# Kernel tuning notes

Measured on AMD Instinct MI355X. Metric: run time of the kernel, lower is better.

The kernel has to match this reference:

```python
import jax, jax.numpy as jnp
import numpy as np
import math

PHI = (1 + math.sqrt(5)) / 2
COMPRESS_EXP = 2.0 / 3.0
ALPHA_D = 0.01


def c_mag(z):
    return jnp.sqrt(z[..., 0] ** 2 + z[..., 1] ** 2 + 1e-08)


def c_phase(z):
    return jnp.arctan2(z[..., 1], z[..., 0] + 1e-10)


def c_mul(a, b):
    real = a[..., 0] * b[..., 0] - a[..., 1] * b[..., 1]
    imag = a[..., 0] * b[..., 1] + a[..., 1] * b[..., 0]
    return jnp.stack([real, imag], axis=-1)


@jax.custom_vjp
def fractal_compress(mag):
    return jnp.clip(mag, 1e-08) ** COMPRESS_EXP


def _fc_fwd(mag):
    ms = jnp.clip(mag, 1e-08)
    c = ms ** COMPRESS_EXP
    return c, c / (ms + 1e-06)


def _fc_bwd(ratio, g):
    return (g * jnp.minimum(ratio, 2.0),)


fractal_compress.defvjp(_fc_fwd, _fc_bwd)


def converge(z):
    mag = c_mag(z)
    phase = c_phase(z)
    cm = fractal_compress(mag)
    return jnp.stack([cm * jnp.cos(phase), cm * jnp.sin(phase)], axis=-1)


def setup_inputs():
    key = jax.random.key(0)
    Bsz, T, D, S = 4, 512, 1024, 16
    dt_rank = D // 16
    ks = jax.random.split(key, 8)
    scale = 1.0 / PHI

    def u(k, shape):
        fan_in = shape[1]
        lim = scale / math.sqrt(fan_in)
        return jax.random.uniform(k, shape, minval=-lim, maxval=lim, dtype=jnp.float32)

    return {
        "x": jax.random.normal(ks[0], (Bsz, T, D), dtype=jnp.float32),
        "W_in": u(ks[1], (2 * D, D)),
        "W_xproj": u(ks[2], (dt_rank + 4 * S, D)),
        "W_dt": u(ks[3], (D, dt_rank)),
        "b_dt": jax.random.uniform(ks[4], (D,), minval=-0.1, maxval=0.1, dtype=jnp.float32),
        "W_out": u(ks[5], (D, D)),
        "b_out": jax.random.uniform(ks[6], (D,), minval=-0.1, maxval=0.1, dtype=jnp.float32),
        "W_res": u(ks[7], (2 * S, D)),
        "A_log": jnp.log(jnp.linspace(1.0, float(S), S)),
    }


def reference(x, W_in, W_xproj, W_dt, b_dt, W_out, b_out, W_res, A_log):
    Bsz, T, D = x.shape
    S = A_log.shape[0]
    dt_rank = W_dt.shape[1]

    xz = x @ W_in.T                      # [B,T,2D]
    x_in, z = xz[..., :D], xz[..., D:]
    x_in = jax.nn.silu(x_in)
    xp = x_in @ W_xproj.T                # [B,T,dt_rank+4S]
    dt = jax.nn.softplus(xp[..., :dt_rank] @ W_dt.T + b_dt)   # [B,T,D]
    bc = xp[..., dt_rank:].reshape(Bsz, T, 2, S, 2)
    B_all, C_all = bc[:, :, 0], bc[:, :, 1]                    # [B,T,S,2]

    A_neg = -jnp.exp(A_log)              # [S]

    # initial deep state d: differentiated phases, tiny magnitude
    phases = jnp.linspace(0.0, 2 * math.pi * (1 - 1.0 / S), S)
    d0 = jnp.stack([0.01 * jnp.cos(phases), 0.01 * jnp.sin(phases)], axis=-1)
    d0 = jnp.broadcast_to(d0, (Bsz, S, 2)).astype(x.dtype)
    h0 = jnp.zeros((Bsz, D, S, 2), dtype=x.dtype)

    def step(carry, xs):
        h_prev, d_prev = carry
        x_t, dt_t, B_t, C_t = xs        # [B,D], [B,D], [B,S,2], [B,S,2]
        x_complex = (x_t @ W_res.T).reshape(Bsz, S, 2)
        d_read = jax.lax.stop_gradient(d_prev)
        T_gate = jnp.cos((c_phase(x_complex) - c_phase(d_read)) / 2) ** 2  # [B,S]
        d_mag = c_mag(d_read)[..., None]
        d_normed = d_read / (d_mag + 1e-08)
        d_scale = jnp.sqrt(jnp.clip(d_mag, 1e-06, 20.0))
        surfaced = d_normed * d_scale * T_gate[..., None]                  # [B,S,2]

        alpha = jnp.exp(dt_t[..., None] * A_neg)                           # [B,D,S]
        x_full = jnp.stack([x_t, jnp.zeros_like(x_t)], axis=-1)            # [B,D,2]
        Bx = c_mul(B_t[:, None, :, :], x_full[:, :, None, :])              # [B,D,S,2]
        Bx = Bx + surfaced[:, None, :, :]
        Bx = Bx * dt_t[:, :, None, None]                                   # gamma scaling

        h_decayed = h_prev * alpha[..., None]
        released = h_prev * (1.0 - alpha)[..., None]
        comp = jnp.clip(converge(released), -10.0, 10.0)
        comp_avg = comp.mean(axis=1)                                       # [B,S,2]
        d_t = jax.lax.stop_gradient(d_prev) + ALPHA_D * comp_avg
        d_mag_new = c_mag(d_t)[..., None]
        d_t = jnp.where(d_mag_new > 20.0, d_t * (20.0 / d_mag_new), d_t)

        h_t = h_decayed + Bx
        Ch = c_mul(C_t[:, None, :, :], h_t)                                # [B,D,S,2]
        y_t = Ch[..., 0].sum(axis=-1)                                      # [B,D]
        return (h_t, d_t), y_t

    xs = (
        jnp.swapaxes(x_in, 0, 1),
        jnp.swapaxes(dt, 0, 1),
        jnp.swapaxes(B_all, 0, 1),
        jnp.swapaxes(C_all, 0, 1),
    )
    (_, _), ys = jax.lax.scan(step, (h0, d0), xs)
    y = jnp.swapaxes(ys, 0, 1)           # [B,T,D]
    y = y * jax.nn.silu(z)
    return y @ W_out.T + b_out
```

## Files before the change

kernel.cpp:

```cpp
#include <hip/hip_runtime.h>
#include <hip/hip_bf16.h>
#include <math.h>


enum { EPI_NONE=0, EPI_SILU=1, EPI_SPBIAS=2, EPI_BIAS=3 };

template<int EPI>
__device__ __forceinline__ float epi_apply(float v, float b) {
  if constexpr (EPI == EPI_SILU)        { return v / (1.0f + expf(-v)); }
  else if constexpr (EPI == EPI_SPBIAS) { float t = v + b; return fmaxf(t, 0.0f) + log1pf(expf(-fabsf(t))); }
  else if constexpr (EPI == EPI_BIAS)   { return v + b; }
  else return v;
}

template<int EPI, bool HAS_A2>
__global__ __launch_bounds__(256) void gemm_wt(
    const float* __restrict__ A, int lda,
    const float* __restrict__ A2, int lda2,
    const float* __restrict__ W, int ldw,
    const float* __restrict__ bias,
    float* __restrict__ C, int ldc,
    int N, int K)
{
  constexpr int BM = 64, BN = 64, BK = 32, PAD = 4;
  __shared__ float As[BK][BM + PAD];
  __shared__ float Ws[BK][BN + PAD];
  const int m0 = blockIdx.x * BM;
  const int n0 = blockIdx.y * BN;
  const int tid = threadIdx.x;
  const int tx = tid & 15;
  const int ty = tid >> 4;
  const int lm = tid & 63;
  const int lk = (tid >> 6) << 3;

  float4 a0, a1, w0, w1;
  {
    const float* p = A + (size_t)(m0 + lm) * lda + lk;
    a0 = ((const float4*)p)[0]; a1 = ((const float4*)p)[1];
    if (HAS_A2) {
      const float* p2 = A2 + (size_t)(m0 + lm) * lda2 + lk;
      const float4 b0 = ((const float4*)p2)[0], b1 = ((const float4*)p2)[1];
      a0.x*=b0.x; a0.y*=b0.y; a0.z*=b0.z; a0.w*=b0.w;
      a1.x*=b1.x; a1.y*=b1.y; a1.z*=b1.z; a1.w*=b1.w;
    }
    const int n = n0 + lm;
    if (n < N) {
      const float* pw = W + (size_t)n * ldw + lk;
      w0 = ((const float4*)pw)[0]; w1 = ((const float4*)pw)[1];
    } else { w0 = make_float4(0.f,0.f,0.f,0.f); w1 = w0; }
  }

  float acc[4][4] = {{0.f,0.f,0.f,0.f},{0.f,0.f,0.f,0.f},{0.f,0.f,0.f,0.f},{0.f,0.f,0.f,0.f}};
  const int NT = K / BK;

  for (int i = 0; i < NT; ++i) {
    __syncthreads();
    As[lk+0][lm]=a0.x; As[lk+1][lm]=a0.y; As[lk+2][lm]=a0.z; As[lk+3][lm]=a0.w;
    As[lk+4][lm]=a1.x; As[lk+5][lm]=a1.y; As[lk+6][lm]=a1.z; As[lk+7][lm]=a1.w;
    Ws[lk+0][lm]=w0.x; Ws[lk+1][lm]=w0.y; Ws[lk+2][lm]=w0.z; Ws[lk+3][lm]=w0.w;
    Ws[lk+4][lm]=w1.x; Ws[lk+5][lm]=w1.y; Ws[lk+6][lm]=w1.z; Ws[lk+7][lm]=w1.w;
    __syncthreads();
    if (i + 1 < NT) {
      const int k0 = (i + 1) * BK;
      const float* p = A + (size_t)(m0 + lm) * lda + k0 + lk;
      a0 = ((const float4*)p)[0]; a1 = ((const float4*)p)[1];
      if (HAS_A2) {
        const float* p2 = A2 + (size_t)(m0 + lm) * lda2 + k0 + lk;
        const float4 b0 = ((const float4*)p2)[0], b1 = ((const float4*)p2)[1];
        a0.x*=b0.x; a0.y*=b0.y; a0.z*=b0.z; a0.w*=b0.w;
        a1.x*=b1.x; a1.y*=b1.y; a1.z*=b1.z; a1.w*=b1.w;
      }
      const int n = n0 + lm;
      if (n < N) {
        const float* pw = W + (size_t)n * ldw + k0 + lk;
        w0 = ((const float4*)pw)[0]; w1 = ((const float4*)pw)[1];
      } else { w0 = make_float4(0.f,0.f,0.f,0.f); w1 = w0; }
    }
#pragma unroll
    for (int kk = 0; kk < BK; ++kk) {
      const float4 a = *(const float4*)&As[kk][ty << 2];
      const float4 w = *(const float4*)&Ws[kk][tx << 2];
      const float ar[4] = {a.x, a.y, a.z, a.w};
      const float wr[4] = {w.x, w.y, w.z, w.w};
#pragma unroll
      for (int ii = 0; ii < 4; ++ii)
#pragma unroll
        for (int j = 0; j < 4; ++j)
          acc[ii][j] = fmaf(ar[ii], wr[j], acc[ii][j]);
    }
  }

  const int ncol = n0 + (tx << 2);
  float bj[4] = {0.f, 0.f, 0.f, 0.f};
  if constexpr (EPI == EPI_SPBIAS || EPI == EPI_BIAS) {
    if (ncol < N) { const float4 bv = *(const float4*)(bias + ncol); bj[0]=bv.x; bj[1]=bv.y; bj[2]=bv.z; bj[3]=bv.w; }
  }
  if (ncol < N) {
#pragma unroll
    for (int i = 0; i < 4; ++i) {
      float vs[4];
#pragma unroll
      for (int j = 0; j < 4; ++j) vs[j] = epi_apply<EPI>(acc[i][j], bj[j]);
      *(float4*)(C + (size_t)(m0 + (ty << 2) + i) * ldc + ncol) = make_float4(vs[0], vs[1], vs[2], vs[3]);
    }
  }
}

__global__ __launch_bounds__(256) void gemm_dualw32(
    const float* __restrict__ A, int lda,
    const float* __restrict__ W1,
    const float* __restrict__ W2, int ldw,
    float* __restrict__ C, int ldc, int K)
{
  constexpr int BM = 32, BN = 32, BK = 32, PAD = 4;
  __shared__ float As[BK][BM + PAD];
  __shared__ float Ws[BK][BN + PAD];
  const int m0 = blockIdx.x * BM;
  const int n0 = blockIdx.y * BN;
  const int tid = threadIdx.x;
  const int tx = tid & 15;
  const int ty = tid >> 4;
  const int lm = tid & 31;
  const int lk = (tid >> 5) << 2;

  const int n = n0 + lm;
  const float* wrow = (n < 128) ? (W1 + (size_t)n * ldw) : (W2 + (size_t)(n - 128) * ldw);

  float4 av = *(const float4*)(A + (size_t)(m0 + lm) * lda + lk);
  float4 wv = *(const float4*)(wrow + lk);

  float acc[2][2] = {{0.f,0.f},{0.f,0.f}};
  const int NT = K / BK;
  for (int i = 0; i < NT; ++i) {
    __syncthreads();
    As[lk+0][lm]=av.x; As[lk+1][lm]=av.y; As[lk+2][lm]=av.z; As[lk+3][lm]=av.w;
    Ws[lk+0][lm]=wv.x; Ws[lk+1][lm]=wv.y; Ws[lk+2][lm]=wv.z; Ws[lk+3][lm]=wv.w;
    __syncthreads();
    if (i + 1 < NT) {
      const int k0 = (i + 1) * BK;
      av = *(const float4*)(A + (size_t)(m0 + lm) * lda + k0 + lk);
      wv = *(const float4*)(wrow + k0 + lk);
    }
#pragma unroll
    for (int kk = 0; kk < BK; ++kk) {
      const float2 a = *(const float2*)&As[kk][ty << 1];
      const float2 w = *(const float2*)&Ws[kk][tx << 1];
      acc[0][0] = fmaf(a.x, w.x, acc[0][0]);
      acc[0][1] = fmaf(a.x, w.y, acc[0][1]);
      acc[1][0] = fmaf(a.y, w.x, acc[1][0]);
      acc[1][1] = fmaf(a.y, w.y, acc[1][1]);
    }
  }
  const int ncol = n0 + (tx << 1);
  float* pc = C + (size_t)(m0 + (ty << 1)) * ldc + ncol;
  *(float2*)pc         = make_float2(acc[0][0], acc[0][1]);
  *(float2*)(pc + ldc) = make_float2(acc[1][0], acc[1][1]);
}

__global__ __launch_bounds__(256) void gemm_dt64(
    const float* __restrict__ A, int lda,
    const float* __restrict__ W,
    const float* __restrict__ bias,
    float* __restrict__ C, int ldc)
{
  __shared__ float As[64][68];
  __shared__ float Ws[64][68];
  const int m0 = blockIdx.x * 64;
  const int n0 = blockIdx.y * 64;
  const int tid = threadIdx.x;
  const int lm = tid & 63;
  const int kq = (tid >> 6) << 4;

  {
    const float* pa = A + (size_t)(m0 + lm) * lda + kq;
    const float4 a0 = ((const float4*)pa)[0];
    const float4 a1 = ((const float4*)pa)[1];
    const float4 a2 = ((const float4*)pa)[2];
    const float4 a3 = ((const float4*)pa)[3];
    const float* pw = W + (size_t)(n0 + lm) * 64 + kq;
    const float4 w0 = ((const float4*)pw)[0];
    const float4 w1 = ((const float4*)pw)[1];
    const float4 w2 = ((const float4*)pw)[2];
    const float4 w3 = ((const float4*)pw)[3];
    As[kq+ 0][lm]=a0.x; As[kq+ 1][lm]=a0.y; As[kq+ 2][lm]=a0.z; As[kq+ 3][lm]=a0.w;
    As[kq+ 4][lm]=a1.x; As[kq+ 5][lm]=a1.y; As[kq+ 6][lm]=a1.z; As[kq+ 7][lm]=a1.w;
    As[kq+ 8][lm]=a2.x; As[kq+ 9][lm]=a2.y; As[kq+10][lm]=a2.z; As[kq+11][lm]=a2.w;
    As[kq+12][lm]=a3.x; As[kq+13][lm]=a3.y; As[kq+14][lm]=a3.z; As[kq+15][lm]=a3.w;
    Ws[kq+ 0][lm]=w0.x; Ws[kq+ 1][lm]=w0.y; Ws[kq+ 2][lm]=w0.z; Ws[kq+ 3][lm]=w0.w;
    Ws[kq+ 4][lm]=w1.x; Ws[kq+ 5][lm]=w1.y; Ws[kq+ 6][lm]=w1.z; Ws[kq+ 7][lm]=w1.w;
    Ws[kq+ 8][lm]=w2.x; Ws[kq+ 9][lm]=w2.y; Ws[kq+10][lm]=w2.z; Ws[kq+11][lm]=w2.w;
    Ws[kq+12][lm]=w3.x; Ws[kq+13][lm]=w3.y; Ws[kq+14][lm]=w3.z; Ws[kq+15][lm]=w3.w;
  }
  __syncthreads();

  const int tx = tid & 15;
  const int ty = tid >> 4;
  float acc[4][4] = {{0.f,0.f,0.f,0.f},{0.f,0.f,0.f,0.f},{0.f,0.f,0.f,0.f},{0.f,0.f,0.f,0.f}};
#pragma unroll 16
  for (int kk = 0; kk < 64; ++kk) {
    const float4 a = *(const float4*)&As[kk][ty << 2];
    const float4 w = *(const float4*)&Ws[kk][tx << 2];
    const float ar[4] = {a.x, a.y, a.z, a.w};
    const float wr[4] = {w.x, w.y, w.z, w.w};
#pragma unroll
    for (int i = 0; i < 4; ++i)
#pragma unroll
      for (int j = 0; j < 4; ++j)
        acc[i][j] = fmaf(ar[i], wr[j], acc[i][j]);
  }

  const int ncol = n0 + (tx << 2);
  const float4 bv = *(const float4*)(bias + ncol);
  const float bj[4] = {bv.x, bv.y, bv.z, bv.w};
#pragma unroll
  for (int i = 0; i < 4; ++i) {
    float vs[4];
#pragma unroll
    for (int j = 0; j < 4; ++j) vs[j] = epi_apply<EPI_SPBIAS>(acc[i][j], bj[j]);
    *(float4*)(C + (size_t)(m0 + (ty << 2) + i) * ldc + ncol) = make_float4(vs[0], vs[1], vs[2], vs[3]);
  }
}

__global__ void zero_kernel(float4* __restrict__ p, int n4) {
  const int i = blockIdx.x * blockDim.x + threadIdx.x;
  if (i < n4) p[i] = make_float4(0.f, 0.f, 0.f, 0.f);
}

__global__ __launch_bounds__(256) void reduce_y_silu(
    const float4* __restrict__ yp, const float* __restrict__ siluxz,
    float4* __restrict__ yo, int n4)
{
  const int i = blockIdx.x * blockDim.x + threadIdx.x;
  if (i >= n4) return;
  float4 a = yp[i];
#pragma unroll
  for (int s = 1; s < 16; ++s) {
    const float4 v = yp[(size_t)s * 524288 + i];
    a.x += v.x; a.y += v.y; a.z += v.z; a.w += v.w;
  }
  const int row = i >> 8;
  const int c4  = i & 255;
  const float4 z = *(const float4*)(siluxz + (size_t)row * 2048 + 1024 + (c4 << 2));
  a.x *= z.x; a.y *= z.y; a.z *= z.z; a.w *= z.w;
  yo[i] = a;
}

__global__ __launch_bounds__(256) void mul_silu(
    float* __restrict__ y, const float* __restrict__ siluxz, int n)
{
  const int i = blockIdx.x * blockDim.x + threadIdx.x;
  if (i >= n) return;
  const int row = i >> 10;
  const int col = i & 1023;
  y[i] *= siluxz[(size_t)row * 2048 + 1024 + col];
}

template<int CTRL>
__device__ __forceinline__ float dpp_fadd(float x) {
  const int s = __builtin_amdgcn_update_dpp(0, __float_as_int(x), CTRL, 0xF, 0xF, true);
  return x + __int_as_float(s);
}
__device__ __forceinline__ float wave64_sum_l63(float x) {
  x = dpp_fadd<0x111>(x);
  x = dpp_fadd<0x112>(x);
  x = dpp_fadd<0x114>(x);
  x = dpp_fadd<0x118>(x);
  x = dpp_fadd<0x142>(x);
  x = dpp_fadd<0x143>(x);
  return x;
}

__device__ __forceinline__ void comp_block(const float4& dtv, const float na2,
    const float (&h_r)[4], const float (&h_i)[4], float (&al_out)[4],
    float& wr, float& wi)
{
  const float ta[4] = {dtv.x, dtv.y, dtv.z, dtv.w};
  float sr = 0.f, si = 0.f;
#pragma unroll
  for (int e = 0; e < 4; ++e) {
    const float a = exp2f(ta[e] * na2);
    al_out[e] = a;
    const float om    = 1.0f - a;
    const float rel_r = h_r[e] * om, rel_i = h_i[e] * om;
    const float m2 = fmaf(rel_r, rel_r, fmaf(rel_i, rel_i, 1e-8f));
    const float u  = exp2f(log2f(m2) * (-1.0f / 6.0f));
    const float rr = rel_r + 1e-10f;
    float cr = rr * u;    cr = fminf(fmaxf(cr, -10.f), 10.f);
    float ci = rel_i * u; ci = fminf(fmaxf(ci, -10.f), 10.f);
    sr += cr; si += ci;
  }
  wr = wave64_sum_l63(sr);
  wi = wave64_sum_l63(si);
}

template<bool PARTIAL>
__device__ __forceinline__ void step_update(
    float& d_r, float& d_i, const float avg_r, const float avg_i,
    const float2& cx, const float4& xv, const float4& dtv,
    const float2& Bv, const float2& Cv,
    const float (&alv)[4], float (&h_r)[4], float (&h_i)[4],
    float* py)
{
  d_r = fmaf(0.01f, avg_r, d_r);
  d_i = fmaf(0.01f, avg_i, d_i);
  const float dm2c = fmaf(d_r, d_r, fmaf(d_i, d_i, 1e-8f));
  if (dm2c > 400.f) { const float sc = 20.f * __builtin_amdgcn_rsqf(dm2c); d_r *= sc; d_i *= sc; }

  const float xr2 = cx.x + 1e-10f;
  const float irx = __builtin_amdgcn_rsqf(fmaf(xr2, xr2, fmaf(cx.y, cx.y, 1e-38f)));
  const float dr2 = d_r + 1e-10f;
  const float ird = __builtin_amdgcn_rsqf(fmaf(dr2, dr2, fmaf(d_i, d_i, 1e-38f)));
  const float cosdp = fmaf(xr2, dr2, cx.y * d_i) * irx * ird;
  const float Tg  = 0.5f * (1.0f + cosdp);
  const float md2 = fmaf(d_r, d_r, fmaf(d_i, d_i, 1e-8f));
  const float sf  = Tg * exp2f(log2f(md2) * -0.25f);
  const float s_r = d_r * sf, s_i = d_i * sf;

  const float xa[4] = {xv.x, xv.y, xv.z, xv.w};
  const float ta[4] = {dtv.x, dtv.y, dtv.z, dtv.w};
  float yv[4];
#pragma unroll
  for (int e = 0; e < 4; ++e) {
    const float bx_r = fmaf(Bv.x, xa[e], s_r) * ta[e];
    const float bx_i = fmaf(Bv.y, xa[e], s_i) * ta[e];
    h_r[e] = fmaf(h_r[e], alv[e], bx_r);
    h_i[e] = fmaf(h_i[e], alv[e], bx_i);
    yv[e] = fmaf(Cv.x, h_r[e], -(Cv.y * h_i[e]));
  }
  if (PARTIAL) {
    *(float4*)py = make_float4(yv[0], yv[1], yv[2], yv[3]);
  } else {
#pragma unroll
    for (int e = 0; e < 4; ++e) atomicAdd(py + e, yv[e]);
  }
}

template<int RB, int RO, bool PARTIAL>
__device__ __forceinline__ void period_body(
    const float* __restrict__ px, const float* __restrict__ pdt,
    const float* __restrict__ pB, const float* __restrict__ pC,
    const float* __restrict__ pxc, float* __restrict__ py,
    const float na2, const int lane, const int wid,
    float (*red)[4][4],
    float& d_r, float& d_i,
    float (&h_r)[4], float (&h_i)[4], float (&al)[4],
    float4& x0, float4& t0, float2& B0, float2& C0, float2& c0,
    float4& x1, float4& t1, float2& B1, float2& C1, float2& c1,
    const float4& t2)
{
  const float4 qa = *(const float4*)&red[RB][0][0];
  const float4 qb = *(const float4*)&red[RB][1][0];
  const float4 qc = *(const float4*)&red[RB][2][0];
  const float4 qd = *(const float4*)&red[RB][3][0];

  step_update<PARTIAL>(d_r, d_i,
      (qa.x + qb.x + qc.x + qd.x) * (1.0f / 1024.0f),
      (qa.y + qb.y + qc.y + qd.y) * (1.0f / 1024.0f),
      c0, x0, t0, B0, C0, al, h_r, h_i, py + (size_t)RO * 1024);

  x0 = *(const float4*)(px  + (size_t)(RO + 3) * 2048);
  t0 = *(const float4*)(pdt + (size_t)(RO + 3) * 1024);
  B0 = *(const float2*)(pB  + (RO + 3) * 160);
  C0 = *(const float2*)(pC  + (RO + 3) * 160);
  c0 = *(const float2*)(pxc + (RO + 3) * 160);

  float al1[4], w1r, w1i;
  comp_block(t1, na2, h_r, h_i, al1, w1r, w1i);

  step_update<PARTIAL>(d_r, d_i,
      (qa.z + qb.z + qc.z + qd.z) * (1.0f / 1024.0f),
      (qa.w + qb.w + qc.w + qd.w) * (1.0f / 1024.0f),
      c1, x1, t1, B1, C1, al1, h_r, h_i, py + (size_t)(RO + 1) * 1024);

  x1 = *(const float4*)(px  + (size_t)(RO + 4) * 2048);
  t1 = *(const float4*)(pdt + (size_t)(RO + 4) * 1024);
  B1 = *(const float2*)(pB  + (RO + 4) * 160);
  C1 = *(const float2*)(pC  + (RO + 4) * 160);
  c1 = *(const float2*)(pxc + (RO + 4) * 160);

  float w2r, w2i;
  comp_block(t2, na2, h_r, h_i, al, w2r, w2i);

  if (lane == 63) *(float4*)&red[(RB + 1) % 3][wid][0] = make_float4(w1r, w1i, w2r, w2i);

  asm volatile("s_waitcnt lgkmcnt(0)" ::: "memory");
  __builtin_amdgcn_s_barrier();
  asm volatile("" ::: "memory");
}

template<bool PARTIAL>
__global__ __launch_bounds__(256) void scan_g1b(
    const float* __restrict__ xin,
    const float* __restrict__ xpc,
    const float* __restrict__ dtb,
    const float* __restrict__ A_log,
    float* __restrict__ ybase,
    int T,
    const float* __restrict__ xg,
    const float* __restrict__ Wz,
    float* __restrict__ Cz)
{
  if (blockIdx.x < 64) {
    __builtin_amdgcn_s_setprio(1);

    const int b = blockIdx.x >> 4;
    const int s = blockIdx.x & 15;
    const int d0 = threadIdx.x << 2;
    const int lane = threadIdx.x & 63;
    const int wid = threadIdx.x >> 6;

    __shared__ __align__(16) float red[3][4][4];

    const float a_s = expf(A_log[s]);
    const float na2 = -a_s * 1.4426950408889634f;
    const float phase = (float)(6.283185307179586 * (double)s / 16.0);
    float d_r = 0.01f * cosf(phase);
    float d_i = 0.01f * sinf(phase);
    float h_r[4] = {0.f,0.f,0.f,0.f};
    float h_i[4] = {0.f,0.f,0.f,0.f};
    float al[4];

    const size_t rb = (size_t)b * T;
    const float* px  = xin + rb * 2048 + d0;
    const float* pdt = dtb + rb * 1024 + d0;
    const float* pB  = xpc + rb * 160 + 64 + 2 * s;
    const float* pC  = xpc + rb * 160 + 96 + 2 * s;
    const float* pxc = xpc + rb * 160 + 128 + 2 * s;
    float* py = PARTIAL ? (ybase + (size_t)s * (4 * 512 * 1024) + rb * 1024 + d0)
                        : (ybase + rb * 1024 + d0);

    float4 xA = *(const float4*)px;
    float4 tA = *(const float4*)pdt;
    float2 BA = *(const float2*)pB;
    float2 CA = *(const float2*)pC;
    float2 cA = *(const float2*)pxc;
    float4 xB = *(const float4*)(px + 2048);
    float4 tB = *(const float4*)(pdt + 1024);
    float2 BB = *(const float2*)(pB + 160);
    float2 CB = *(const float2*)(pC + 160);
    float2 cB = *(const float2*)(pxc + 160);
    float4 xC = *(const float4*)(px + 2 * 2048);
    float4 tC = *(const float4*)(pdt + 2 * 1024);
    float2 BC = *(const float2*)(pB + 2 * 160);
    float2 CC = *(const float2*)(pC + 2 * 160);
    float2 cC = *(const float2*)(pxc + 2 * 160);

    {
      float w0r, w0i;
      comp_block(tA, na2, h_r, h_i, al, w0r, w0i);
      if (lane == 63) *(float4*)&red[0][wid][0] = make_float4(0.f, 0.f, w0r, w0i);
    }
    __syncthreads();

    for (int it = 0; it < 85; ++it) {
      period_body<0, 0, PARTIAL>(px, pdt, pB, pC, pxc, py, na2, lane, wid, red,
          d_r, d_i, h_r, h_i, al,
          xA, tA, BA, CA, cA,  xB, tB, BB, CB, cB,  tC);
      period_body<1, 2, PARTIAL>(px, pdt, pB, pC, pxc, py, na2, lane, wid, red,
          d_r, d_i, h_r, h_i, al,
          xC, tC, BC, CC, cC,  xA, tA, BA, CA, cA,  tB);
      period_body<2, 4, PARTIAL>(px, pdt, pB, pC, pxc, py, na2, lane, wid, red,
          d_r, d_i, h_r, h_i, al,
          xB, tB, BB, CB, cB,  xC, tC, BC, CC, cC,  tA);
      px += 6 * 2048; pdt += 6 * 1024; pB += 6 * 160; pC += 6 * 160; pxc += 6 * 160;
      py += 6 * 1024;
    }
    period_body<0, 0, PARTIAL>(px, pdt, pB, pC, pxc, py, na2, lane, wid, red,
        d_r, d_i, h_r, h_i, al,
        xA, tA, BA, CA, cA,  xB, tB, BB, CB, cB,  tC);
    __builtin_amdgcn_s_setprio(0);
  } else {
    constexpr int BK = 32, PAD = 4;
    __shared__ float As[BK][64 + PAD];
    __shared__ float Ws[BK][64 + PAD];
    const int b2 = blockIdx.x - 64;
    const int m0 = (b2 & 31) << 6;
    const int n0 = (b2 >> 5) << 6;
    const int tid = threadIdx.x;
    const int tx = tid & 15;
    const int ty = tid >> 4;
    const int lm = tid & 63;
    const int lk = (tid >> 6) << 3;

    float4 a0, a1, w0, w1;
    {
      const float* p = xg + (size_t)(m0 + lm) * 1024 + lk;
      a0 = ((const float4*)p)[0]; a1 = ((const float4*)p)[1];
      const float* pw = Wz + (size_t)(n0 + lm) * 1024 + lk;
      w0 = ((const float4*)pw)[0]; w1 = ((const float4*)pw)[1];
    }
    float acc[4][4] = {{0.f,0.f,0.f,0.f},{0.f,0.f,0.f,0.f},{0.f,0.f,0.f,0.f},{0.f,0.f,0.f,0.f}};
    const int NT = 1024 / BK;
    for (int i = 0; i < NT; ++i) {
      __syncthreads();
      As[lk+0][lm]=a0.x; As[lk+1][lm]=a0.y; As[lk+2][lm]=a0.z; As[lk+3][lm]=a0.w;
      As[lk+4][lm]=a1.x; As[lk+5][lm]=a1.y; As[lk+6][lm]=a1.z; As[lk+7][lm]=a1.w;
      Ws[lk+0][lm]=w0.x; Ws[lk+1][lm]=w0.y; Ws[lk+2][lm]=w0.z; Ws[lk+3][lm]=w0.w;
      Ws[lk+4][lm]=w1.x; Ws[lk+5][lm]=w1.y; Ws[lk+6][lm]=w1.z; Ws[lk+7][lm]=w1.w;
      __syncthreads();
      if (i + 1 < NT) {
        const int k0 = (i + 1) * BK;
        const float* p = xg + (size_t)(m0 + lm) * 1024 + k0 + lk;
        a0 = ((const float4*)p)[0]; a1 = ((const float4*)p)[1];
        const float* pw = Wz + (size_t)(n0 + lm) * 1024 + k0 + lk;
        w0 = ((const float4*)pw)[0]; w1 = ((const float4*)pw)[1];
      }
#pragma unroll
      for (int kk = 0; kk < BK; ++kk) {
        const float4 a = *(const float4*)&As[kk][ty << 2];
        const float4 w = *(const float4*)&Ws[kk][tx << 2];
        const float ar[4] = {a.x, a.y, a.z, a.w};
        const float wr[4] = {w.x, w.y, w.z, w.w};
#pragma unroll
        for (int ii = 0; ii < 4; ++ii)
#pragma unroll
          for (int j = 0; j < 4; ++j)
            acc[ii][j] = fmaf(ar[ii], wr[j], acc[ii][j]);
      }
    }
    const int ncol = n0 + (tx << 2);
#pragma unroll
    for (int i = 0; i < 4; ++i) {
      float vs[4];
#pragma unroll
      for (int j = 0; j < 4; ++j) vs[j] = epi_apply<EPI_SILU>(acc[i][j], 0.f);
      *(float4*)(Cz + (size_t)(m0 + (ty << 2) + i) * 2048 + ncol) = make_float4(vs[0], vs[1], vs[2], vs[3]);
    }
  }
}

extern "C" void kernel_launch(void* const* d_in, const int* in_sizes, int n_in,
                              void* d_out, int out_size, void* d_ws, size_t ws_size,
                              hipStream_t stream) {
  const float* x     = (const float*)d_in[0];
  const float* W_in  = (const float*)d_in[1];
  const float* W_xp  = (const float*)d_in[2];
  const float* W_dt  = (const float*)d_in[3];
  const float* b_dt  = (const float*)d_in[4];
  const float* W_out = (const float*)d_in[5];
  const float* b_out = (const float*)d_in[6];
  const float* W_res = (const float*)d_in[7];
  const float* A_log = (const float*)d_in[8];
  float* out = (float*)d_out;

  float* ws     = (float*)d_ws;
  float* siluxz = ws;
  float* xpc    = siluxz + (size_t)2048 * 2048;
  float* dtb    = xpc    + (size_t)2048 * 160;
  float* ybuf   = dtb    + (size_t)2048 * 1024;
  float* ypart  = ybuf   + (size_t)2048 * 1024;

  const size_t need_bytes = ((size_t)8716288 + (size_t)33554432) * 4;
  const bool use_part = ws_size >= need_bytes;

  gemm_wt<EPI_SILU, false><<<dim3(32, 16), 256, 0, stream>>>(
      x, 1024, nullptr, 0, W_in, 1024, nullptr, siluxz, 2048, 1024, 1024);
  gemm_dualw32<<<dim3(64, 5), 256, 0, stream>>>(
      siluxz, 2048, W_xp, W_res, 1024, xpc, 160, 1024);
  gemm_dt64<<<dim3(32, 16), 256, 0, stream>>>(
      xpc, 160, W_dt, b_dt, dtb, 1024);

  if (use_part) {
    scan_g1b<true><<<dim3(64 + 512), dim3(256), 0, stream>>>(
        siluxz, xpc, dtb, A_log, ypart, 512,
        x, W_in + (size_t)1024 * 1024, siluxz + 1024);
    reduce_y_silu<<<dim3(2048), 256, 0, stream>>>(
        (const float4*)ypart, siluxz, (float4*)ybuf, 524288);
  } else {
    zero_kernel<<<dim3(2048), 256, 0, stream>>>((float4*)ybuf, (2048 * 1024) / 4);
    scan_g1b<false><<<dim3(64 + 512), dim3(256), 0, stream>>>(
        siluxz, xpc, dtb, A_log, ybuf, 512,
        x, W_in + (size_t)1024 * 1024, siluxz + 1024);
    mul_silu<<<dim3(8192), 256, 0, stream>>>(ybuf, siluxz, 2048 * 1024);
  }

  gemm_wt<EPI_BIAS, false><<<dim3(32, 16), 256, 0, stream>>>(
      ybuf, 1024, nullptr, 0, W_out, 1024, b_out, out, 1024, 1024, 1024);
}
```

Measured before the change: 490.1 us.

## Persist z-GEMM blocks in scan kernel and double GEMM K-tile

Result: no change. 498.6 us (+1.7%).

```diff
diff --git a/kernel.cpp b/kernel.cpp
--- a/kernel.cpp
+++ b/kernel.cpp
@@ -13,16 +13,15 @@
   else return v;
 }
 
-template<int EPI, bool HAS_A2>
+template<int EPI>
 __global__ __launch_bounds__(256) void gemm_wt(
     const float* __restrict__ A, int lda,
-    const float* __restrict__ A2, int lda2,
     const float* __restrict__ W, int ldw,
     const float* __restrict__ bias,
     float* __restrict__ C, int ldc,
     int N, int K)
 {
-  constexpr int BM = 64, BN = 64, BK = 32, PAD = 4;
+  constexpr int BM = 64, BN = 64, BK = 64, PAD = 4;
   __shared__ float As[BK][BM + PAD];
   __shared__ float Ws[BK][BN + PAD];
   const int m0 = blockIdx.x * BM;
@@ -31,23 +30,16 @@
   const int tx = tid & 15;
   const int ty = tid >> 4;
   const int lm = tid & 63;
-  const int lk = (tid >> 6) << 3;
-
-  float4 a0, a1, w0, w1;
+  const int lk = (tid >> 6) << 4;
+
+  float4 a0, a1, a2, a3, w0, w1, w2, w3;
   {
     const float* p = A + (size_t)(m0 + lm) * lda + lk;
     a0 = ((const float4*)p)[0]; a1 = ((const float4*)p)[1];
-    if (HAS_A2) {
-      const float* p2 = A2 + (size_t)(m0 + lm) * lda2 + lk;
-      const float4 b0 = ((const float4*)p2)[0], b1 = ((const float4*)p2)[1];
-      a0.x*=b0.x; a0.y*=b0.y; a0.z*=b0.z; a0.w*=b0.w;
-      a1.x*=b1.x; a1.y*=b1.y; a1.z*=b1.z; a1.w*=b1.w;
-    }
-    const int n = n0 + lm;
-    if (n < N) {
-      const float* pw = W + (size_t)n * ldw + lk;
-      w0 = ((const float4*)pw)[0]; w1 = ((const float4*)pw)[1];
-    } else { w0 = make_float4(0.f,0.f,0.f,0.f); w1 = w0; }
+    a2 = ((const float4*)p)[2]; a3 = ((const float4*)p)[3];
+    const float* pw = W + (size_t)(n0 + lm) * ldw + lk;
+    w0 = ((const float4*)pw)[0]; w1 = ((const float4*)pw)[1];
+    w2 = ((const float4*)pw)[2]; w3 = ((const float4*)pw)[3];
   }
 
   float acc[4][4] = {{0.f,0.f,0.f,0.f},{0.f,0.f,0.f,0.f},{0.f,0.f,0.f,0.f},{0.f,0.f,0.f,0.f}};
@@ -55,26 +47,23 @@
 
   for (int i = 0; i < NT; ++i) {
     __syncthreads();
-    As[lk+0][lm]=a0.x; As[lk+1][lm]=a0.y; As[lk+2][lm]=a0.z; As[lk+3][lm]=a0.w;
-    As[lk+4][lm]=a1.x; As[lk+5][lm]=a1.y; As[lk+6][lm]=a1.z; As[lk+7][lm]=a1.w;
-    Ws[lk+0][lm]=w0.x; Ws[lk+1][lm]=w0.y; Ws[lk+2][lm]=w0.z; Ws[lk+3][lm]=w0.w;
-    Ws[lk+4][lm]=w1.x; Ws[lk+5][lm]=w1.y; Ws[lk+6][lm]=w1.z; Ws[lk+7][lm]=w1.w;
+    As[lk+ 0][lm]=a0.x; As[lk+ 1][lm]=a0.y; As[lk+ 2][lm]=a0.z; As[lk+ 3][lm]=a0.w;
+    As[lk+ 4][lm]=a1.x; As[lk+ 5][lm]=a1.y; As[lk+ 6][lm]=a1.z; As[lk+ 7][lm]=a1.w;
+    As[lk+ 8][lm]=a2.x; As[lk+ 9][lm]=a2.y; As[lk+10][lm]=a2.z; As[lk+11][lm]=a2.w;
+    As[lk+12][lm]=a3.x; As[lk+13][lm]=a3.y; As[lk+14][lm]=a3.z; As[lk+15][lm]=a3.w;
+    Ws[lk+ 0][lm]=w0.x; Ws[lk+ 1][lm]=w0.y; Ws[lk+ 2][lm]=w0.z; Ws[lk+ 3][lm]=w0.w;
+    Ws[lk+ 4][lm]=w1.x; Ws[lk+ 5][lm]=w1.y; Ws[lk+ 6][lm]=w1.z; Ws[lk+ 7][lm]=w1.w;
+    Ws[lk+ 8][lm]=w2.x; Ws[lk+ 9][lm]=w2.y; Ws[lk+10][lm]=w2.z; Ws[lk+11][lm]=w2.w;
+    Ws[lk+12][lm]=w3.x; Ws[lk+13][lm]=w3.y; Ws[lk+14][lm]=w3.z; Ws[lk+15][lm]=w3.w;
     __syncthreads();
     if (i + 1 < NT) {
       const int k0 = (i + 1) * BK;
       const float* p = A + (size_t)(m0 + lm) * lda + k0 + lk;
       a0 = ((const float4*)p)[0]; a1 = ((const float4*)p)[1];
-      if (HAS_A2) {
-        const float* p2 = A2 + (size_t)(m0 + lm) * lda2 + k0 + lk;
-        const float4 b0 = ((const float4*)p2)[0], b1 = ((const float4*)p2)[1];
-        a0.x*=b0.x; a0.y*=b0.y; a0.z*=b0.z; a0.w*=b0.w;
-        a1.x*=b1.x; a1.y*=b1.y; a1.z*=b1.z; a1.w*=b1.w;
-      }
-      const int n = n0 + lm;
-      if (n < N) {
-        const float* pw = W + (size_t)n * ldw + k0 + lk;
-        w0 = ((const float4*)pw)[0]; w1 = ((const float4*)pw)[1];
-      } else { w0 = make_float4(0.f,0.f,0.f,0.f); w1 = w0; }
+      a2 = ((const float4*)p)[2]; a3 = ((const float4*)p)[3];
+      const float* pw = W + (size_t)(n0 + lm) * ldw + k0 + lk;
+      w0 = ((const float4*)pw)[0]; w1 = ((const float4*)pw)[1];
+      w2 = ((const float4*)pw)[2]; w3 = ((const float4*)pw)[3];
     }
 #pragma unroll
     for (int kk = 0; kk < BK; ++kk) {
@@ -93,16 +82,15 @@
   const int ncol = n0 + (tx << 2);
   float bj[4] = {0.f, 0.f, 0.f, 0.f};
   if constexpr (EPI == EPI_SPBIAS || EPI == EPI_BIAS) {
-    if (ncol < N) { const float4 bv = *(const float4*)(bias + ncol); bj[0]=bv.x; bj[1]=bv.y; bj[2]=bv.z; bj[3]=bv.w; }
-  }
-  if (ncol < N) {
-#pragma unroll
-    for (int i = 0; i < 4; ++i) {
-      float vs[4];
-#pragma unroll
-      for (int j = 0; j < 4; ++j) vs[j] = epi_apply<EPI>(acc[i][j], bj[j]);
-      *(float4*)(C + (size_t)(m0 + (ty << 2) + i) * ldc + ncol) = make_float4(vs[0], vs[1], vs[2], vs[3]);
-    }
+    const float4 bv = *(const float4*)(bias + ncol);
+    bj[0]=bv.x; bj[1]=bv.y; bj[2]=bv.z; bj[3]=bv.w;
+  }
+#pragma unroll
+  for (int i = 0; i < 4; ++i) {
+    float vs[4];
+#pragma unroll
+    for (int j = 0; j < 4; ++j) vs[j] = epi_apply<EPI>(acc[i][j], bj[j]);
+    *(float4*)(C + (size_t)(m0 + (ty << 2) + i) * ldc + ncol) = make_float4(vs[0], vs[1], vs[2], vs[3]);
   }
 }
 
@@ -473,58 +461,62 @@
     constexpr int BK = 32, PAD = 4;
     __shared__ float As[BK][64 + PAD];
     __shared__ float Ws[BK][64 + PAD];
-    const int b2 = blockIdx.x - 64;
-    const int m0 = (b2 & 31) << 6;
-    const int n0 = (b2 >> 5) << 6;
+    const int bg = blockIdx.x - 64;
     const int tid = threadIdx.x;
     const int tx = tid & 15;
     const int ty = tid >> 4;
     const int lm = tid & 63;
     const int lk = (tid >> 6) << 3;
 
-    float4 a0, a1, w0, w1;
-    {
-      const float* p = xg + (size_t)(m0 + lm) * 1024 + lk;
-      a0 = ((const float4*)p)[0]; a1 = ((const float4*)p)[1];
-      const float* pw = Wz + (size_t)(n0 + lm) * 1024 + lk;
-      w0 = ((const float4*)pw)[0]; w1 = ((const float4*)pw)[1];
-    }
-    float acc[4][4] = {{0.f,0.f,0.f,0.f},{0.f,0.f,0.f,0.f},{0.f,0.f,0.f,0.f},{0.f,0.f,0.f,0.f}};
-    const int NT = 1024 / BK;
-    for (int i = 0; i < NT; ++i) {
-      __syncthreads();
-      As[lk+0][lm]=a0.x; As[lk+1][lm]=a0.y; As[lk+2][lm]=a0.z; As[lk+3][lm]=a0.w;
-      As[lk+4][lm]=a1.x; As[lk+5][lm]=a1.y; As[lk+6][lm]=a1.z; As[lk+7][lm]=a1.w;
-      Ws[lk+0][lm]=w0.x; Ws[lk+1][lm]=w0.y; Ws[lk+2][lm]=w0.z; Ws[lk+3][lm]=w0.w;
-      Ws[lk+4][lm]=w1.x; Ws[lk+5][lm]=w1.y; Ws[lk+6][lm]=w1.z; Ws[lk+7][lm]=w1.w;
-      __syncthreads();
-      if (i + 1 < NT) {
-        const int k0 = (i + 1) * BK;
-        const float* p = xg + (size_t)(m0 + lm) * 1024 + k0 + lk;
+    for (int t2 = bg; t2 < 512; t2 += 192) {
+      const int m0 = (t2 & 31) << 6;
+      const int n0 = (t2 >> 5) << 6;
+
+      float4 a0, a1, w0, w1;
+      {
+        const float* p = xg + (size_t)(m0 + lm) * 1024 + lk;
         a0 = ((const float4*)p)[0]; a1 = ((const float4*)p)[1];
-        const float* pw = Wz + (size_t)(n0 + lm) * 1024 + k0 + lk;
+        const float* pw = Wz + (size_t)(n0 + lm) * 1024 + lk;
         w0 = ((const float4*)pw)[0]; w1 = ((const float4*)pw)[1];
       }
-#pragma unroll
-      for (int kk = 0; kk < BK; ++kk) {
-        const float4 a = *(const float4*)&As[kk][ty << 2];
-        const float4 w = *(const float4*)&Ws[kk][tx << 2];
-        const float ar[4] = {a.x, a.y, a.z, a.w};
-        const float wr[4] = {w.x, w.y, w.z, w.w};
-#pragma unroll
-        for (int ii = 0; ii < 4; ++ii)
-#pragma unroll
-          for (int j = 0; j < 4; ++j)
-            acc[ii][j] = fmaf(ar[ii], wr[j], acc[ii][j]);
+      float acc[4][4] = {{0.f,0.f,0.f,0.f},{0.f,0.f,0.f,0.f},{0.f,0.f,0.f,0.f},{0.f,0.f,0.f,0.f}};
+      const int NT = 1024 / BK;
+      for (int i = 0; i < NT; ++i) {
+        __syncthreads();
+        As[lk+0][lm]=a0.x; As[lk+1][lm]=a0.y; As[lk+2][lm]=a0.z; As[lk+3][lm]=a0.w;
+        As[lk+4][lm]=a1.x; As[lk+5][lm]=a1.y; As[lk+6][lm]=a1.z; As[lk+7][lm]=a1.w;
+        Ws[lk+0][lm]=w0.x; Ws[lk+1][lm]=w0.y; Ws[lk+2][lm]=w0.z; Ws[lk+3][lm]=w0.w;
+        Ws[lk+4][lm]=w1.x; Ws[lk+5][lm]=w1.y; Ws[lk+6][lm]=w1.z; Ws[lk+7][lm]=w1.w;
+        __syncthreads();
+        if (i + 1 < NT) {
+          const int k0 = (i + 1) * BK;
+          const float* p = xg + (size_t)(m0 + lm) * 1024 + k0 + lk;
+          a0 = ((const float4*)p)[0]; a1 = ((const float4*)p)[1];
+          const float* pw = Wz + (size_t)(n0 + lm) * 1024 + k0 + lk;
+          w0 = ((const float4*)pw)[0]; w1 = ((const float4*)pw)[1];
+        }
+#pragma unroll
+        for (int kk = 0; kk < BK; ++kk) {
+          const float4 a = *(const float4*)&As[kk][ty << 2];
+          const float4 w = *(const float4*)&Ws[kk][tx << 2];
+          const float ar[4] = {a.x, a.y, a.z, a.w};
+          const float wr[4] = {w.x, w.y, w.z, w.w};
+#pragma unroll
+          for (int ii = 0; ii < 4; ++ii)
+#pragma unroll
+            for (int j = 0; j < 4; ++j)
+              acc[ii][j] = fmaf(ar[ii], wr[j], acc[ii][j]);
+        }
       }
-    }
-    const int ncol = n0 + (tx << 2);
-#pragma unroll
-    for (int i = 0; i < 4; ++i) {
-      float vs[4];
-#pragma unroll
-      for (int j = 0; j < 4; ++j) vs[j] = epi_apply<EPI_SILU>(acc[i][j], 0.f);
-      *(float4*)(Cz + (size_t)(m0 + (ty << 2) + i) * 2048 + ncol) = make_float4(vs[0], vs[1], vs[2], vs[3]);
+      const int ncol = n0 + (tx << 2);
+#pragma unroll
+      for (int i = 0; i < 4; ++i) {
+        float vs[4];
+#pragma unroll
+        for (int j = 0; j < 4; ++j) vs[j] = epi_apply<EPI_SILU>(acc[i][j], 0.f);
+        *(float4*)(Cz + (size_t)(m0 + (ty << 2) + i) * 2048 + ncol) = make_float4(vs[0], vs[1], vs[2], vs[3]);
+      }
+      __syncthreads();
     }
   }
 }
@@ -553,27 +545,27 @@
   const size_t need_bytes = ((size_t)8716288 + (size_t)33554432) * 4;
   const bool use_part = ws_size >= need_bytes;
 
-  gemm_wt<EPI_SILU, false><<<dim3(32, 16), 256, 0, stream>>>(
-      x, 1024, nullptr, 0, W_in, 1024, nullptr, siluxz, 2048, 1024, 1024);
+  gemm_wt<EPI_SILU><<<dim3(32, 16), 256, 0, stream>>>(
+      x, 1024, W_in, 1024, nullptr, siluxz, 2048, 1024, 1024);
   gemm_dualw32<<<dim3(64, 5), 256, 0, stream>>>(
       siluxz, 2048, W_xp, W_res, 1024, xpc, 160, 1024);
   gemm_dt64<<<dim3(32, 16), 256, 0, stream>>>(
       xpc, 160, W_dt, b_dt, dtb, 1024);
 
   if (use_part) {
-    scan_g1b<true><<<dim3(64 + 512), dim3(256), 0, stream>>>(
+    scan_g1b<true><<<dim3(256), dim3(256), 0, stream>>>(
         siluxz, xpc, dtb, A_log, ypart, 512,
         x, W_in + (size_t)1024 * 1024, siluxz + 1024);
     reduce_y_silu<<<dim3(2048), 256, 0, stream>>>(
         (const float4*)ypart, siluxz, (float4*)ybuf, 524288);
   } else {
     zero_kernel<<<dim3(2048), 256, 0, stream>>>((float4*)ybuf, (2048 * 1024) / 4);
-    scan_g1b<false><<<dim3(64 + 512), dim3(256), 0, stream>>>(
+    scan_g1b<false><<<dim3(256), dim3(256), 0, stream>>>(
         siluxz, xpc, dtb, A_log, ybuf, 512,
         x, W_in + (size_t)1024 * 1024, siluxz + 1024);
     mul_silu<<<dim3(8192), 256, 0, stream>>>(ybuf, siluxz, 2048 * 1024);
   }
 
-  gemm_wt<EPI_BIAS, false><<<dim3(32, 16), 256, 0, stream>>>(
-      ybuf, 1024, nullptr, 0, W_out, 1024, b_out, out, 1024, 1024, 1024);
-}
+  gemm_wt<EPI_BIAS><<<dim3(32, 16), 256, 0, stream>>>(
+      ybuf, 1024, W_out, 1024, b_out, out, 1024, 1024, 1024);
+}
```
